# Kernel optimization log

Hardware: AMD Instinct MI355X
Metric: run time of the kernel (lower is better)

Reference implementation:

```python
import jax, jax.numpy as jnp
import numpy as np

BOUND = 2.0


def _near_far_cube(rays_o, rays_d, bound):
    tmin = (-bound - rays_o) / (rays_d + 1e-15)
    tmax = (bound - rays_o) / (rays_d + 1e-15)
    near = jnp.max(jnp.minimum(tmin, tmax), axis=-1, keepdims=True)
    far = jnp.min(jnp.maximum(tmin, tmax), axis=-1, keepdims=True)
    bad = far < near
    near = jnp.where(bad, 1e9, near)
    far = jnp.where(bad, 1e9, far)
    near = jnp.maximum(near, 0.05)
    return near, far


def _sample_pdf_det(bins, weights, n_samples):
    # bins: [R, M], weights: [R, M-1]  (deterministic / eval-mode u)
    weights = weights + 1e-5
    pdf = weights / jnp.sum(weights, -1, keepdims=True)
    cdf = jnp.cumsum(pdf, -1)
    cdf = jnp.concatenate([jnp.zeros_like(cdf[:, :1]), cdf], -1)  # [R, M]
    u = jnp.linspace(0.5 / n_samples, 1.0 - 0.5 / n_samples, n_samples, dtype=cdf.dtype)
    u = jnp.broadcast_to(u, (cdf.shape[0], n_samples))
    inds = jax.vmap(lambda c, uu: jnp.searchsorted(c, uu, side='right'))(cdf, u)
    below = jnp.maximum(inds - 1, 0)
    above = jnp.minimum(inds, cdf.shape[-1] - 1)
    cdf_b = jnp.take_along_axis(cdf, below, -1)
    cdf_a = jnp.take_along_axis(cdf, above, -1)
    bins_b = jnp.take_along_axis(bins, below, -1)
    bins_a = jnp.take_along_axis(bins, above, -1)
    denom = cdf_a - cdf_b
    denom = jnp.where(denom < 1e-5, jnp.ones_like(denom), denom)
    t = (u - cdf_b) / denom
    return bins_b + t * (bins_a - bins_b)


def _field(pts, dirs, W1, b1, W2, b2, Wsig, Wrgb, brgb):
    # stand-in NeRF field (base class is abstract): tiny MLP
    h = jax.nn.relu(pts @ W1 + b1)
    h = jax.nn.relu(h @ W2 + b2)
    sigma = jax.nn.softplus((h @ Wsig)[..., 0])
    rgb = jax.nn.sigmoid(jnp.concatenate([h, dirs], -1) @ Wrgb + brgb)
    return sigma, rgb


def _composite_weights(z_vals, sigmas, sample_dist):
    deltas = z_vals[..., 1:] - z_vals[..., :-1]
    deltas = jnp.concatenate([deltas, jnp.broadcast_to(sample_dist, deltas[..., :1].shape)], -1)
    alphas = 1.0 - jnp.exp(-deltas * sigmas)
    shifted = jnp.concatenate([jnp.ones_like(alphas[..., :1]), 1.0 - alphas + 1e-15], -1)
    weights = alphas * jnp.cumprod(shifted, -1)[..., :-1]
    return weights, deltas


def _run(rays_o, rays_d, W1, b1, W2, b2, Wsig, Wrgb, brgb, num_steps, upsample_steps):
    B, N = rays_o.shape[:2]
    near, far = _near_far_cube(rays_o, rays_d, BOUND)          # [B,N,1]
    z = jnp.linspace(0.0, 1.0, num_steps, dtype=rays_o.dtype)
    z_vals = near + (far - near) * z                            # [B,N,S]
    sample_dist = (far - near) / num_steps                      # [B,N,1]
    pts = jnp.clip(rays_o[..., None, :] + rays_d[..., None, :] * z_vals[..., None], -BOUND, BOUND)
    dirs = jnp.broadcast_to(rays_d[..., None, :], pts.shape)
    sigmas, rgbs = _field(pts, dirs, W1, b1, W2, b2, Wsig, Wrgb, brgb)  # [B,N,S], [B,N,S,3]

    # importance resampling (no_grad + detach in torch -> stop_gradient)
    w, deltas = _composite_weights(z_vals, sigmas, sample_dist)
    z_mid = z_vals[..., :-1] + 0.5 * deltas[..., :-1]           # [B,N,S-1]
    new_z = _sample_pdf_det(z_mid.reshape(B * N, -1), w.reshape(B * N, -1)[:, 1:-1], upsample_steps)
    new_z = jax.lax.stop_gradient(new_z).reshape(B, N, upsample_steps)
    new_pts = jnp.clip(rays_o[..., None, :] + rays_d[..., None, :] * new_z[..., None], -BOUND, BOUND)
    new_dirs = jnp.broadcast_to(rays_d[..., None, :], new_pts.shape)
    new_sigmas, new_rgbs = _field(new_pts, new_dirs, W1, b1, W2, b2, Wsig, Wrgb, brgb)

    # merge coarse + fine samples, sort along ray
    z_all = jnp.concatenate([z_vals, new_z], -1)                # [B,N,S+U]
    idx = jnp.argsort(z_all, axis=-1)
    z_all = jnp.take_along_axis(z_all, idx, -1)
    sig_all = jnp.take_along_axis(jnp.concatenate([sigmas, new_sigmas], -1), idx, -1)
    rgb_all = jnp.take_along_axis(jnp.concatenate([rgbs, new_rgbs], -2), idx[..., None], -2)

    w, _ = _composite_weights(z_all, sig_all, sample_dist)
    weights_sum = jnp.sum(w, -1)                                # [B,N]
    ori_z = jnp.clip((z_all - near) / (far - near), 0.0, 1.0)
    depth = jnp.sum(w * ori_z, -1)                              # [B,N]
    image = jnp.sum(w[..., None] * rgb_all, -2)                 # [B,N,3]
    image = image + (1.0 - weights_sum)[..., None] * 1.0        # bg_color = 1
    return depth, image


def setup_inputs() -> dict:
    key = jax.random.key(0)
    ks = jax.random.split(key, 8)
    B, N, H = 1, 4096, 64
    rays_o = jax.random.normal(ks[0], (B, N, 3), jnp.float32) * 0.5
    rays_d = jax.random.normal(ks[1], (B, N, 3), jnp.float32)
    rays_d = rays_d / jnp.linalg.norm(rays_d, axis=-1, keepdims=True)
    return {
        'rays_o': rays_o,
        'rays_d': rays_d,
        'W1': jax.random.normal(ks[2], (3, H), jnp.float32) / np.sqrt(3.0),
        'b1': jnp.zeros((H,), jnp.float32),
        'W2': jax.random.normal(ks[3], (H, H), jnp.float32) / np.sqrt(H),
        'b2': jnp.zeros((H,), jnp.float32),
        'Wsig': jax.random.normal(ks[4], (H, 1), jnp.float32) / np.sqrt(H),
        'Wrgb': jax.random.normal(ks[5], (H + 3, 3), jnp.float32) / np.sqrt(H + 3),
        'brgb': jnp.zeros((3,), jnp.float32),
        'num_steps': 128,
        'upsample_steps': 128,
    }


def reference(rays_o, rays_d, W1, b1, W2, b2, Wsig, Wrgb, brgb, num_steps, upsample_steps):
    return _run(rays_o, rays_d, W1, b1, W2, b2, Wsig, Wrgb, brgb, num_steps, upsample_steps)
```

## Files before the change

kernel.cpp:

```cpp
#include <hip/hip_runtime.h>
#include <math.h>


#define BOUNDF 2.0f

typedef _Float16 f16;
typedef f16 f16x2 __attribute__((ext_vector_type(2)));
typedef f16 f16x8 __attribute__((ext_vector_type(8)));
typedef float f32x4 __attribute__((ext_vector_type(4)));

union U16 { f16x8 v8; f16x2 v2[4]; };

struct __align__(16) RayLds {
    float zf[128];
    float cdf[128];
    f32x4 rgbc4[128];
    f32x4 rgbf4[128];
    f32x4 stg[128];
    unsigned short perm[256];
};

__device__ __forceinline__ f32x4 mfma16(f16x8 a, f16x8 b, f32x4 c) {
    return __builtin_amdgcn_mfma_f32_16x16x32_f16(a, b, c, 0, 0, 0);
}

__device__ __forceinline__ f16x2 pkrtz(float a, float b) {
    return __builtin_bit_cast(f16x2, __builtin_amdgcn_cvt_pkrtz(a, b));
}

__device__ __forceinline__ f16x8 relu_pk(f16x8 x) {
    const f16x8 z = {(f16)0.f, (f16)0.f, (f16)0.f, (f16)0.f,
                     (f16)0.f, (f16)0.f, (f16)0.f, (f16)0.f};
    return __builtin_elementwise_max(x, z);
}

__device__ __forceinline__ float scan_incl_mul(float p, int lane) {
#pragma unroll
    for (int off = 1; off < 64; off <<= 1) {
        float t = __shfl_up(p, off, 64);
        if (lane >= off) p *= t;
    }
    return p;
}

__device__ __forceinline__ float scan_incl_add(float p, int lane) {
#pragma unroll
    for (int off = 1; off < 64; off <<= 1) {
        float t = __shfl_up(p, off, 64);
        if (lane >= off) p += t;
    }
    return p;
}

__device__ __forceinline__ void cvt_relu2(
    f32x4 a0, f32x4 a1, f32x4 a2, f32x4 a3, f16x8& f0, f16x8& f1)
{
    U16 u0, u1;
    u0.v2[0] = pkrtz(a0[0], a0[1]);
    u0.v2[1] = pkrtz(a0[2], a0[3]);
    u0.v2[2] = pkrtz(a1[0], a1[1]);
    u0.v2[3] = pkrtz(a1[2], a1[3]);
    u1.v2[0] = pkrtz(a2[0], a2[1]);
    u1.v2[1] = pkrtz(a2[2], a2[3]);
    u1.v2[2] = pkrtz(a3[0], a3[1]);
    u1.v2[3] = pkrtz(a3[2], a3[3]);
    f0 = relu_pk(u0.v8);
    f1 = relu_pk(u1.v8);
}

template<bool COARSE>
__device__ __forceinline__ void field_pass(
    RayLds& R,
    f16x8 w1a0, f16x8 w1a1, f16x8 w1a2, f16x8 w1a3,
    f16x8 b00, f16x8 b01, f16x8 b10, f16x8 b11,
    f16x8 b20, f16x8 b21, f16x8 b30, f16x8 b31,
    f16x8 hda0, f16x8 hda1,
    f32x4 b2q0, f32x4 b2q1, f32x4 b2q2, f32x4 b2q3,
    float ox, float oy, float oz, float dx, float dy, float dzv,
    float nearv, float span, float base_r, float base_g, float base_b, int lane)
{
    const int ms = lane & 15;
    const f32x4 zero = {0.f, 0.f, 0.f, 0.f};
    U16 upA, upB;
    upA.v2[2] = f16x2{(f16)0.f, (f16)0.f};
    upA.v2[3] = f16x2{(f16)0.f, (f16)0.f};
    upB.v2[2] = f16x2{(f16)0.f, (f16)0.f};
    upB.v2[3] = f16x2{(f16)0.f, (f16)0.f};
#pragma unroll 1
    for (int Mtb = 0; Mtb < 2; ++Mtb) {
#pragma unroll 1
        for (int half = 0; half < 2; ++half) {
            const int mA = Mtb * 64 + (half * 2 + 0) * 16 + ms;
            const int mB = Mtb * 64 + (half * 2 + 1) * 16 + ms;
            float zA = COARSE ? fmaf(span, (float)mA * (1.0f / 127.0f), nearv) : R.zf[mA];
            float zB = COARSE ? fmaf(span, (float)mB * (1.0f / 127.0f), nearv) : R.zf[mB];
            float pxA = fminf(fmaxf(fmaf(dx, zA, ox), -BOUNDF), BOUNDF);
            float pyA = fminf(fmaxf(fmaf(dy, zA, oy), -BOUNDF), BOUNDF);
            float pzA = fminf(fmaxf(fmaf(dzv, zA, oz), -BOUNDF), BOUNDF);
            float pxB = fminf(fmaxf(fmaf(dx, zB, ox), -BOUNDF), BOUNDF);
            float pyB = fminf(fmaxf(fmaf(dy, zB, oy), -BOUNDF), BOUNDF);
            float pzB = fminf(fmaxf(fmaf(dzv, zB, oz), -BOUNDF), BOUNDF);
            upA.v2[0] = pkrtz(pxA, pyA);
            upA.v2[1] = pkrtz(pzA, 1.0f);
            upB.v2[0] = pkrtz(pxB, pyB);
            upB.v2[1] = pkrtz(pzB, 1.0f);
            f16x8 pfA = upA.v8, pfB = upB.v8;

            f32x4 hA0 = mfma16(w1a0, pfA, zero);
            f32x4 hB0 = mfma16(w1a0, pfB, zero);
            f32x4 hA1 = mfma16(w1a1, pfA, zero);
            f32x4 hB1 = mfma16(w1a1, pfB, zero);
            f32x4 hA2 = mfma16(w1a2, pfA, zero);
            f32x4 hB2 = mfma16(w1a2, pfB, zero);
            f32x4 hA3 = mfma16(w1a3, pfA, zero);
            f32x4 hB3 = mfma16(w1a3, pfB, zero);

            f16x8 hfA0, hfA1, hfB0, hfB1;
            cvt_relu2(hA0, hA1, hA2, hA3, hfA0, hfA1);
            cvt_relu2(hB0, hB1, hB2, hB3, hfB0, hfB1);

            f32x4 iA0 = mfma16(b00, hfA0, b2q0);
            f32x4 iB0 = mfma16(b00, hfB0, b2q0);
            f32x4 iA1 = mfma16(b10, hfA0, b2q1);
            f32x4 iB1 = mfma16(b10, hfB0, b2q1);
            f32x4 iA2 = mfma16(b20, hfA0, b2q2);
            f32x4 iB2 = mfma16(b20, hfB0, b2q2);
            f32x4 iA3 = mfma16(b30, hfA0, b2q3);
            f32x4 iB3 = mfma16(b30, hfB0, b2q3);
            f32x4 aA0 = mfma16(b01, hfA1, iA0);
            f32x4 aB0 = mfma16(b01, hfB1, iB0);
            f32x4 aA1 = mfma16(b11, hfA1, iA1);
            f32x4 aB1 = mfma16(b11, hfB1, iB1);
            f32x4 aA2 = mfma16(b21, hfA1, iA2);
            f32x4 aB2 = mfma16(b21, hfB1, iB2);
            f32x4 aA3 = mfma16(b31, hfA1, iA3);
            f32x4 aB3 = mfma16(b31, hfB1, iB3);

            f16x8 gA0, gA1, gB0, gB1;
            cvt_relu2(aA0, aA1, aA2, aA3, gA0, gA1);
            cvt_relu2(aB0, aB1, aB2, aB3, gB0, gB1);

            f32x4 jA = mfma16(hda0, gA0, zero);
            f32x4 jB = mfma16(hda0, gB0, zero);
            f32x4 tvA = mfma16(hda1, gA1, jA);
            f32x4 tvB = mfma16(hda1, gB1, jB);

            if (lane < 16) {
                R.stg[mA] = tvA;
                R.stg[mB] = tvB;
            }
        }
        {
            f32x4 tq = R.stg[Mtb * 64 + lane];
            int m2 = Mtb * 64 + lane;
            float e  = __expf(-fabsf(tq[0]));
            float sg = fmaxf(tq[0], 0.0f) + __logf(1.0f + e);
            float rr = __builtin_amdgcn_rcpf(1.0f + __expf(-(tq[1] + base_r)));
            float gg = __builtin_amdgcn_rcpf(1.0f + __expf(-(tq[2] + base_g)));
            float bb = __builtin_amdgcn_rcpf(1.0f + __expf(-(tq[3] + base_b)));
            f32x4 o = {rr, gg, bb, sg};
            if (COARSE) R.rgbc4[m2] = o; else R.rgbf4[m2] = o;
        }
    }
}

__global__ __launch_bounds__(256)
void nerf_kernel(const float* __restrict__ rays_o, const float* __restrict__ rays_d,
                 const float* __restrict__ W1, const float* __restrict__ b1,
                 const float* __restrict__ W2, const float* __restrict__ b2,
                 const float* __restrict__ Wsig, const float* __restrict__ Wrgb,
                 const float* __restrict__ brgb,
                 float* __restrict__ out_depth, float* __restrict__ out_img,
                 int nRays)
{
    __shared__ RayLds rl[4];

    const int tid  = threadIdx.x;
    const int lane = tid & 63;
    const int wv   = tid >> 6;
    const int ms   = lane & 15;
    const int quad = lane >> 4;

    f16x8 w1a[4];
#pragma unroll
    for (int nt = 0; nt < 4; ++nt) {
        f16x8 t;
#pragma unroll
        for (int j = 0; j < 8; ++j) t[j] = (f16)0.f;
        if (quad == 0) {
            int u = 32 * (nt >> 1) + 8 * (ms >> 2) + 4 * (nt & 1) + (ms & 3);
            t[0] = (f16)W1[u];
            t[1] = (f16)W1[64 + u];
            t[2] = (f16)W1[128 + u];
            t[3] = (f16)b1[u];
        }
        w1a[nt] = t;
    }

    const int colbase = 8 * (ms >> 2) + (ms & 3);
    f16x8 b00, b01, b10, b11, b20, b21, b30, b31;
#pragma unroll
    for (int j = 0; j < 8; ++j) {
        int k0 = (quad * 8 + j) * 64;
        int k1 = (32 + quad * 8 + j) * 64;
        b00[j] = (f16)W2[k0 + colbase];      b01[j] = (f16)W2[k1 + colbase];
        b10[j] = (f16)W2[k0 + colbase + 4];  b11[j] = (f16)W2[k1 + colbase + 4];
        b20[j] = (f16)W2[k0 + colbase + 32]; b21[j] = (f16)W2[k1 + colbase + 32];
        b30[j] = (f16)W2[k0 + colbase + 36]; b31[j] = (f16)W2[k1 + colbase + 36];
    }
    f32x4 b2q0, b2q1, b2q2, b2q3;
#pragma unroll
    for (int r = 0; r < 4; ++r) {
        b2q0[r] = b2[8 * quad + r];
        b2q1[r] = b2[8 * quad + 4 + r];
        b2q2[r] = b2[32 + 8 * quad + r];
        b2q3[r] = b2[32 + 8 * quad + 4 + r];
    }
    f16x8 hda0, hda1;
    {
        int msel = ms & 3;
#pragma unroll
        for (int j = 0; j < 8; ++j) {
            int u0 = quad * 8 + j, u1 = 32 + quad * 8 + j;
            float w0 = (msel == 0) ? Wsig[u0] : Wrgb[u0 * 3 + msel - 1];
            float w1 = (msel == 0) ? Wsig[u1] : Wrgb[u1 * 3 + msel - 1];
            hda0[j] = (f16)w0;
            hda1[j] = (f16)w1;
        }
    }

    int ray = blockIdx.x * 4 + wv;
    bool valid = ray < nRays;
    int rayc = valid ? ray : (nRays - 1);
    RayLds& R = rl[wv];

    const float ox = rays_o[rayc * 3 + 0], oy = rays_o[rayc * 3 + 1], oz = rays_o[rayc * 3 + 2];
    const float dx = rays_d[rayc * 3 + 0], dy = rays_d[rayc * 3 + 1], dzv = rays_d[rayc * 3 + 2];

    float t0x = (-BOUNDF - ox) / (dx + 1e-15f), t1x = (BOUNDF - ox) / (dx + 1e-15f);
    float t0y = (-BOUNDF - oy) / (dy + 1e-15f), t1y = (BOUNDF - oy) / (dy + 1e-15f);
    float t0z = (-BOUNDF - oz) / (dzv + 1e-15f), t1z = (BOUNDF - oz) / (dzv + 1e-15f);
    float nearv = fmaxf(fminf(t0x, t1x), fmaxf(fminf(t0y, t1y), fminf(t0z, t1z)));
    float farv  = fminf(fmaxf(t0x, t1x), fminf(fmaxf(t0y, t1y), fmaxf(t0z, t1z)));
    if (farv < nearv) { nearv = 1e9f; farv = 1e9f; }
    nearv = fmaxf(nearv, 0.05f);
    const float span = farv - nearv;
    const float dzc = span * (1.0f / 127.0f);
    const float sample_dist = span * (1.0f / 128.0f);

    const float base_r = brgb[0] + dx * Wrgb[64 * 3 + 0] + dy * Wrgb[65 * 3 + 0] + dzv * Wrgb[66 * 3 + 0];
    const float base_g = brgb[1] + dx * Wrgb[64 * 3 + 1] + dy * Wrgb[65 * 3 + 1] + dzv * Wrgb[66 * 3 + 1];
    const float base_b = brgb[2] + dx * Wrgb[64 * 3 + 2] + dy * Wrgb[65 * 3 + 2] + dzv * Wrgb[66 * 3 + 2];

    field_pass<true>(R, w1a[0], w1a[1], w1a[2], w1a[3],
                     b00, b01, b10, b11, b20, b21, b30, b31,
                     hda0, hda1, b2q0, b2q1, b2q2, b2q3,
                     ox, oy, oz, dx, dy, dzv, nearv, span, base_r, base_g, base_b, lane);

    {
        float sgA = R.rgbc4[2 * lane][3];
        float sgB = R.rgbc4[2 * lane + 1][3];
        float aA = 1.0f - __expf(-dzc * sgA);
        float dB = (lane == 63) ? sample_dist : dzc;
        float aB = 1.0f - __expf(-dB * sgB);
        float mA = 1.0f - aA + 1e-15f, mB = 1.0f - aB + 1e-15f;
        float pp = scan_incl_mul(mA * mB, lane);
        float T0 = __shfl_up(pp, 1, 64);
        if (lane == 0) T0 = 1.0f;
        float w0 = aA * T0;
        float w1 = aB * (T0 * mA);
        float w2n = __shfl_down(w0, 1, 64);
        float pA = w1 + 1e-5f;
        float pB = w2n + 1e-5f;
        if (lane == 63) { pA = 0.f; pB = 0.f; }
        float S = scan_incl_add(pA + pB, lane);
        float total = __shfl(S, 63, 64);
        float sexcl = __shfl_up(S, 1, 64);
        if (lane == 0) sexcl = 0.f;
        float inv = 1.0f / total;
        if (lane == 63) {
            R.cdf[0] = 0.0f;
        } else {
            R.cdf[1 + 2 * lane] = (sexcl + pA) * inv;
            R.cdf[2 + 2 * lane] = (sexcl + pA + pB) * inv;
        }
    }

#pragma unroll
    for (int bt = 0; bt < 2; ++bt) {
        int i = bt * 64 + lane;
        float u = (float)(2 * i + 1) * (1.0f / 256.0f);
        int lo = 0, hi = 127;
#pragma unroll
        for (int it = 0; it < 7; ++it) {
            int mid = (lo + hi) >> 1;
            if (R.cdf[mid] <= u) lo = mid + 1; else hi = mid;
        }
        int below = max(lo - 1, 0), above = min(lo, 126);
        float cb = R.cdf[below], ca = R.cdf[above];
        float binb = fmaf(dzc, (float)below + 0.5f, nearv);
        float bina = fmaf(dzc, (float)above + 0.5f, nearv);
        float denom = ca - cb;
        if (denom < 1e-5f) denom = 1.0f;
        float t = (u - cb) / denom;
        R.zf[i] = fmaf(t, bina - binb, binb);
    }

    field_pass<false>(R, w1a[0], w1a[1], w1a[2], w1a[3],
                      b00, b01, b10, b11, b20, b21, b30, b31,
                      hda0, hda1, b2q0, b2q1, b2q2, b2q3,
                      ox, oy, oz, dx, dy, dzv, nearv, span, base_r, base_g, base_b, lane);

#pragma unroll
    for (int bt = 0; bt < 2; ++bt) {
        int k = bt * 64 + lane;
        float v  = fmaf(span, (float)k * (1.0f / 127.0f), nearv);
        float vf = R.zf[k];
        int lo = 0, hi = 128;
        int lo2 = 0, hi2 = 128;
#pragma unroll
        for (int it = 0; it < 8; ++it) {
            if (lo < hi) {
                int mid = (lo + hi) >> 1;
                if (R.zf[mid] < v) lo = mid + 1; else hi = mid;
            }
            if (lo2 < hi2) {
                int mid = (lo2 + hi2) >> 1;
                float zcm = fmaf(span, (float)mid * (1.0f / 127.0f), nearv);
                if (zcm <= vf) lo2 = mid + 1; else hi2 = mid;
            }
        }
        R.perm[k + lo]  = (unsigned short)k;
        R.perm[k + lo2] = (unsigned short)(128 + k);
    }

    {
        int sb = 4 * lane;
        int idxk[4]; float zk[4]; f32x4 ck[4];
#pragma unroll
        for (int k = 0; k < 4; ++k) {
            int idx = R.perm[sb + k];
            idxk[k] = idx;
            float zfv = R.zf[idx & 127];
            float zcv = fmaf(span, (float)idx * (1.0f / 127.0f), nearv);
            zk[k] = (idx < 128) ? zcv : zfv;
            const f32x4* src = (idx < 128) ? &R.rgbc4[idx] : &R.rgbf4[idx - 128];
            ck[k] = *src;
        }
        float znext = __shfl_down(zk[0], 1, 64);
        float d0 = zk[1] - zk[0];
        float d1 = zk[2] - zk[1];
        float d2 = zk[3] - zk[2];
        float d3 = (lane < 63) ? (znext - zk[3]) : sample_dist;
        float a0 = 1.0f - __expf(-d0 * ck[0][3]);
        float a1 = 1.0f - __expf(-d1 * ck[1][3]);
        float a2 = 1.0f - __expf(-d2 * ck[2][3]);
        float a3 = 1.0f - __expf(-d3 * ck[3][3]);
        float m0 = 1.0f - a0 + 1e-15f, m1 = 1.0f - a1 + 1e-15f;
        float m2 = 1.0f - a2 + 1e-15f, m3 = 1.0f - a3 + 1e-15f;
        float p = scan_incl_mul((m0 * m1) * (m2 * m3), lane);
        float T = __shfl_up(p, 1, 64);
        if (lane == 0) T = 1.0f;

        const float invspan = 1.0f / span;
        float dacc = 0.f, racc = 0.f, gacc = 0.f, bacc = 0.f, wacc = 0.f;
        float aarr[4] = {a0, a1, a2, a3};
        float marr[4] = {m0, m1, m2, m3};
#pragma unroll
        for (int k = 0; k < 4; ++k) {
            float w = aarr[k] * T;
            float ozv = (zk[k] - nearv) * invspan;
            ozv = (ozv < 0.0f) ? 0.0f : ((ozv > 1.0f) ? 1.0f : ozv);
            dacc = fmaf(w, ozv, dacc);
            racc = fmaf(w, ck[k][0], racc);
            gacc = fmaf(w, ck[k][1], gacc);
            bacc = fmaf(w, ck[k][2], bacc);
            wacc += w;
            T *= marr[k];
        }
#pragma unroll
        for (int off = 32; off; off >>= 1) {
            dacc += __shfl_xor(dacc, off);
            racc += __shfl_xor(racc, off);
            gacc += __shfl_xor(gacc, off);
            bacc += __shfl_xor(bacc, off);
            wacc += __shfl_xor(wacc, off);
        }
        if (lane == 0 && valid) {
            out_depth[ray] = dacc;
            float bg = 1.0f - wacc;
            out_img[ray * 3 + 0] = racc + bg;
            out_img[ray * 3 + 1] = gacc + bg;
            out_img[ray * 3 + 2] = bacc + bg;
        }
    }
}

extern "C" void kernel_launch(void* const* d_in, const int* in_sizes, int n_in,
                              void* d_out, int out_size, void* d_ws, size_t ws_size,
                              hipStream_t stream) {
    const float* rays_o = (const float*)d_in[0];
    const float* rays_d = (const float*)d_in[1];
    const float* W1   = (const float*)d_in[2];
    const float* b1   = (const float*)d_in[3];
    const float* W2   = (const float*)d_in[4];
    const float* b2   = (const float*)d_in[5];
    const float* Wsig = (const float*)d_in[6];
    const float* Wrgb = (const float*)d_in[7];
    const float* brgb = (const float*)d_in[8];

    int N = in_sizes[0] / 3;
    float* out = (float*)d_out;
    float* out_depth = out;
    float* out_img   = out + N;

    int blocks = (N + 3) / 4;
    nerf_kernel<<<dim3(blocks), dim3(256), 0, stream>>>(
        rays_o, rays_d, W1, b1, W2, b2, Wsig, Wrgb, brgb,
        out_depth, out_img, N);
}
```

Measured before the change: 97.35 us.

## Replace binary searches with histogram-and-scan rank computation for pdf sampling and merge

Replaces the per-sample binary search over the CDF in LDS with a closed-form bucket index per CDF entry, LDS atomic histogram counts and a wave prefix scan to get searchsorted indices. The needed CDF values then come from shuffles, so the CDF array in LDS is dropped. The merge of coarse and fine samples now uses one closed-form search over the uniform coarse grid, plus a histogram scan in place of the second binary search. This removes dependent LDS reads in loops but adds LDS atomics and ties exactness to floating-point rounding in the closed-form bucket computation.

After: 96.88 us. No clear change (-0.5%).

```diff
diff --git a/kernel.cpp b/kernel.cpp
--- a/kernel.cpp
+++ b/kernel.cpp
@@ -13,11 +13,11 @@
 
 struct __align__(16) RayLds {
     float zf[128];
-    float cdf[128];
     f32x4 rgbc4[128];
     f32x4 rgbf4[128];
     f32x4 stg[128];
     unsigned short perm[256];
+    int cnt[128];
 };
 
 __device__ __forceinline__ f32x4 mfma16(f16x8 a, f16x8 b, f32x4 c) {
@@ -50,6 +50,32 @@
         if (lane >= off) p += t;
     }
     return p;
+}
+
+__device__ __forceinline__ int scan_incl_add_i(int p, int lane) {
+#pragma unroll
+    for (int off = 1; off < 64; off <<= 1) {
+        int t = __shfl_up(p, off, 64);
+        if (lane >= off) p += t;
+    }
+    return p;
+}
+
+__device__ __forceinline__ int i0_exact(float c) {
+    float h = 0.5f * (256.0f * c - 1.0f);
+    int v = (int)ceilf(h);
+    return v < 0 ? 0 : (v > 128 ? 128 : v);
+}
+
+__device__ __forceinline__ int count_zc_le(float vf, float span, float nearv) {
+    int lo = 0, hi = 128;
+#pragma unroll
+    for (int it = 0; it < 7; ++it) {
+        int mid = (lo + hi) >> 1;
+        float zcm = fmaf(span, (float)mid * (1.0f / 127.0f), nearv);
+        if (zcm <= vf) lo = mid + 1; else hi = mid;
+    }
+    return lo;
 }
 
 __device__ __forceinline__ void cvt_relu2(
@@ -257,6 +283,7 @@
                      hda0, hda1, b2q0, b2q1, b2q2, b2q3,
                      ox, oy, oz, dx, dy, dzv, nearv, span, base_r, base_g, base_b, lane);
 
+    float zfA, zfB;
     {
         float sgA = R.rgbc4[2 * lane][3];
         float sgB = R.rgbc4[2 * lane + 1][3];
@@ -278,32 +305,50 @@
         float sexcl = __shfl_up(S, 1, 64);
         if (lane == 0) sexcl = 0.f;
         float inv = 1.0f / total;
-        if (lane == 63) {
-            R.cdf[0] = 0.0f;
+        float cdfv1 = (sexcl + pA) * inv;
+        float cdfv2 = (sexcl + pA + pB) * inv;
+
+        R.cnt[lane] = 0;
+        R.cnt[64 + lane] = 0;
+        int i0A = i0_exact(cdfv1);
+        int i0B = i0_exact(cdfv2);
+        if (lane < 63) {
+            if (i0A < 128) atomicAdd(&R.cnt[i0A], 1);
+            if (i0B < 128) atomicAdd(&R.cnt[i0B], 1);
         } else {
-            R.cdf[1 + 2 * lane] = (sexcl + pA) * inv;
-            R.cdf[2 + 2 * lane] = (sexcl + pA + pB) * inv;
-        }
-    }
-
-#pragma unroll
-    for (int bt = 0; bt < 2; ++bt) {
-        int i = bt * 64 + lane;
-        float u = (float)(2 * i + 1) * (1.0f / 256.0f);
-        int lo = 0, hi = 127;
-#pragma unroll
-        for (int it = 0; it < 7; ++it) {
-            int mid = (lo + hi) >> 1;
-            if (R.cdf[mid] <= u) lo = mid + 1; else hi = mid;
-        }
-        int below = max(lo - 1, 0), above = min(lo, 126);
-        float cb = R.cdf[below], ca = R.cdf[above];
-        float binb = fmaf(dzc, (float)below + 0.5f, nearv);
-        float bina = fmaf(dzc, (float)above + 0.5f, nearv);
-        float denom = ca - cb;
-        if (denom < 1e-5f) denom = 1.0f;
-        float t = (u - cb) / denom;
-        R.zf[i] = fmaf(t, bina - binb, binb);
+            atomicAdd(&R.cnt[0], 1);
+        }
+        int cA = R.cnt[2 * lane], cB = R.cnt[2 * lane + 1];
+        int Sc = scan_incl_add_i(cA + cB, lane);
+        int sxc = __shfl_up(Sc, 1, 64);
+        if (lane == 0) sxc = 0;
+        int indsA = sxc + cA;
+        int indsB = Sc;
+
+#pragma unroll
+        for (int bt = 0; bt < 2; ++bt) {
+            int i = bt * 64 + lane;
+            int si = bt * 32 + (lane >> 1);
+            int iA = __shfl(indsA, si, 64);
+            int iB = __shfl(indsB, si, 64);
+            int inds = (lane & 1) ? iB : iA;
+            float u = (float)(2 * i + 1) * (1.0f / 256.0f);
+            int below = max(inds - 1, 0), above = min(inds, 126);
+            int hb = max(below - 1, 0) >> 1;
+            float cb1 = __shfl(cdfv1, hb, 64), cb2 = __shfl(cdfv2, hb, 64);
+            float cb = (below == 0) ? 0.0f : ((below & 1) ? cb1 : cb2);
+            int ha = max(above - 1, 0) >> 1;
+            float ca1 = __shfl(cdfv1, ha, 64), ca2 = __shfl(cdfv2, ha, 64);
+            float ca = (above == 0) ? 0.0f : ((above & 1) ? ca1 : ca2);
+            float binb = fmaf(dzc, (float)below + 0.5f, nearv);
+            float bina = fmaf(dzc, (float)above + 0.5f, nearv);
+            float denom = ca - cb;
+            if (denom < 1e-5f) denom = 1.0f;
+            float t = (u - cb) / denom;
+            float z = fmaf(t, bina - binb, binb);
+            R.zf[i] = z;
+            if (bt == 0) zfA = z; else zfB = z;
+        }
     }
 
     field_pass<false>(R, w1a[0], w1a[1], w1a[2], w1a[3],
@@ -311,27 +356,24 @@
                       hda0, hda1, b2q0, b2q1, b2q2, b2q3,
                       ox, oy, oz, dx, dy, dzv, nearv, span, base_r, base_g, base_b, lane);
 
-#pragma unroll
-    for (int bt = 0; bt < 2; ++bt) {
-        int k = bt * 64 + lane;
-        float v  = fmaf(span, (float)k * (1.0f / 127.0f), nearv);
-        float vf = R.zf[k];
-        int lo = 0, hi = 128;
-        int lo2 = 0, hi2 = 128;
-#pragma unroll
-        for (int it = 0; it < 8; ++it) {
-            if (lo < hi) {
-                int mid = (lo + hi) >> 1;
-                if (R.zf[mid] < v) lo = mid + 1; else hi = mid;
-            }
-            if (lo2 < hi2) {
-                int mid = (lo2 + hi2) >> 1;
-                float zcm = fmaf(span, (float)mid * (1.0f / 127.0f), nearv);
-                if (zcm <= vf) lo2 = mid + 1; else hi2 = mid;
-            }
-        }
-        R.perm[k + lo]  = (unsigned short)k;
-        R.perm[k + lo2] = (unsigned short)(128 + k);
+    {
+        int lo2A = count_zc_le(zfA, span, nearv);
+        int lo2B = count_zc_le(zfB, span, nearv);
+        R.perm[lane + lo2A]      = (unsigned short)(128 + lane);
+        R.perm[64 + lane + lo2B] = (unsigned short)(192 + lane);
+        R.cnt[lane] = 0;
+        R.cnt[64 + lane] = 0;
+        if (lo2A < 128) atomicAdd(&R.cnt[lo2A], 1);
+        if (lo2B < 128) atomicAdd(&R.cnt[lo2B], 1);
+        int cA = R.cnt[2 * lane], cB = R.cnt[2 * lane + 1];
+        int Sc = scan_incl_add_i(cA + cB, lane);
+        int sxc = __shfl_up(Sc, 1, 64);
+        if (lane == 0) sxc = 0;
+        int invA = sxc + cA;
+        int invB = Sc;
+        int k0 = 2 * lane, k1 = 2 * lane + 1;
+        R.perm[k0 + invA] = (unsigned short)k0;
+        R.perm[k1 + invB] = (unsigned short)k1;
     }
 
     {
```
